# Kernel tuning notes

Hardware: AMD Instinct MI355X
Metric: run time of the kernel (lower is better)

## Reference

```python
import jax, jax.numpy as jnp
import numpy as np

# Graph geometry: L depth levels of M nodes, fan_in K scalar connections, per-node dim D
L, M, K, D, B = 8, 128, 32, 16, 2048
N = L * M  # 1024 nodes


def setup_inputs() -> dict:
    key = jax.random.key(0)
    ks = jax.random.split(key, 6)
    x = jax.random.normal(ks[0], (B, D), jnp.float32)
    trace = jax.random.normal(ks[1], (N, B, D), jnp.float32)  # previous-step recurrent state per node
    src_node = jax.random.randint(ks[2], (N, K), 0, N + 1)    # 0 = external input x, else node id (1..N)
    src_feat = jax.random.randint(ks[3], (N, K), 0, D)        # scalar index k within source output
    W = jax.random.normal(ks[4], (N, D, K), jnp.float32) / np.sqrt(K)  # per-node Linear(K -> D)
    b = jax.random.normal(ks[5], (N, D), jnp.float32) * 0.01
    return {"x": x, "trace": trace, "src_node": src_node, "src_feat": src_feat, "W": W, "b": b}


def reference(x, trace, src_node, src_feat, W, b):
    # state buffers have row 0 = external input x, rows 1..N = node states
    h_state = jnp.concatenate([jnp.zeros((1, B, D), x.dtype), jax.lax.stop_gradient(trace)], axis=0)  # prev-step snapshot (detached, like torch .detach())
    cur0 = jnp.concatenate([x[None], jax.lax.stop_gradient(trace)], axis=0)  # current-step buffer, row 0 readable as input
    sn = src_node.reshape(L, M, K)
    sf = src_feat.reshape(L, M, K)
    Wl = W.reshape(L, M, D, K)
    bl = b.reshape(L, M, D)

    def step(cur, xs):
        l, sn_l, sf_l, W_l, b_l = xs
        g_cur = cur[sn_l, :, sf_l]      # [M, K, B] gather from current-step buffer
        g_h = h_state[sn_l, :, sf_l]    # [M, K, B] gather from previous-step snapshot
        # source depth >= current depth -> recurrent edge -> read h; else feedforward -> read cur
        use_h = (sn_l > 0) & (((sn_l - 1) // M) >= l)
        g = jnp.where(use_h[:, :, None], g_h, g_cur)                     # [M, K, B]
        o = jax.nn.relu(jnp.einsum('mkb,mdk->mbd', g, W_l) + b_l[:, None, :])  # [M, B, D]
        cur = jax.lax.dynamic_update_slice(cur, o, (1 + l * M, 0, 0))    # scatter into trace buffer
        return cur, o

    _, outs = jax.lax.scan(step, cur0, (jnp.arange(L), sn, sf, Wl, bl))  # outs: [L, M, B, D]
    return outs.reshape(N, B, D)  # updated trace; last node's forward return is outs[-1]
```

## Files before the change

kernel.cpp:

```cpp
#include <hip/hip_runtime.h>
#include <hip/hip_bf16.h>

#define L_ 8
#define M_ 128
#define K_ 32
#define D_ 16
#define B_ 2048
#define N_ 1024
#define SLAB_ 32768

__global__ __launch_bounds__(256) void transpose_bd(const float* __restrict__ trace,
                                                    const float* __restrict__ x,
                                                    float* __restrict__ traceT,
                                                    float* __restrict__ xT) {
    int blk = blockIdx.x;
    const float* src;
    float* dst;
    int bt;
    if (blk < N_ * 32) {
        int n = blk >> 5;
        src = trace + (size_t)n * SLAB_;
        dst = traceT + (size_t)n * SLAB_;
        bt  = blk & 31;
    } else {
        src = x;
        dst = xT;
        bt  = blk - N_ * 32;
    }
    int b0 = bt * 64;

    __shared__ float lds[D_][65];

    int tid = threadIdx.x;

    const float4* s4 = (const float4*)src;
    int b  = tid >> 2;
    int dq = tid & 3;
    float4 v = s4[(size_t)(b0 + b) * 4 + dq];
    lds[dq * 4 + 0][b] = v.x;
    lds[dq * 4 + 1][b] = v.y;
    lds[dq * 4 + 2][b] = v.z;
    lds[dq * 4 + 3][b] = v.w;
    __syncthreads();

    int d  = tid >> 4;
    int bq = tid & 15;
    float4 w;
    w.x = lds[d][bq * 4 + 0];
    w.y = lds[d][bq * 4 + 1];
    w.z = lds[d][bq * 4 + 2];
    w.w = lds[d][bq * 4 + 3];
    ((float4*)(dst + (size_t)d * B_ + b0))[bq] = w;
}

__global__ __launch_bounds__(256) void layer_kernel(
    int l,
    const float* __restrict__ xbuf, int xfs, int xbs,
    const float* __restrict__ tbuf, int tfs, int tbs,
    const float* __restrict__ obuf, int ofs, int obs,
    const int* __restrict__ sn, const int* __restrict__ sf,
    const float* __restrict__ W, const float* __restrict__ bias,
    float* __restrict__ out, float* __restrict__ outT, int writeT)
{
    int m  = blockIdx.x >> 3;
    int bt = blockIdx.x & 7;
    int n  = l * M_ + m;
    int b  = bt * 256 + threadIdx.x;

    __shared__ float        Wsh[D_][K_];
    __shared__ float        bsh[D_];
    __shared__ const float* colp[K_];
    __shared__ int          colbs[K_];
    __shared__ float        osh[256][17];

    int tid = threadIdx.x;

    if (tid < 128) {
        ((float4*)&Wsh[0][0])[tid] = ((const float4*)(W + (size_t)n * D_ * K_))[tid];
    }
    if (tid < D_) bsh[tid] = bias[(size_t)n * D_ + tid];
    if (tid < K_) {
        int s = sn[(size_t)n * K_ + tid];
        int f = sf[(size_t)n * K_ + tid];
        const float* p;
        int bs;
        if (s == 0) {
            p  = xbuf + (size_t)f * xfs;
            bs = xbs;
        } else {
            int ls = (s - 1) >> 7;
            if (ls >= l) {
                p  = tbuf + (size_t)(s - 1) * SLAB_ + (size_t)f * tfs;
                bs = tbs;
            } else {
                p  = obuf + (size_t)(s - 1) * SLAB_ + (size_t)f * ofs;
                bs = obs;
            }
        }
        colp[tid]  = p;
        colbs[tid] = bs;
    }
    __syncthreads();

    float g[K_];
#pragma unroll
    for (int k = 0; k < K_; ++k) {
        g[k] = colp[k][(size_t)b * colbs[k]];
    }

#pragma unroll
    for (int d = 0; d < D_; ++d) {
        float acc = bsh[d];
#pragma unroll
        for (int k = 0; k < K_; ++k) acc = fmaf(g[k], Wsh[d][k], acc);
        acc = fmaxf(acc, 0.0f);
        osh[tid][d] = acc;
        if (writeT) outT[(size_t)n * SLAB_ + (size_t)d * B_ + b] = acc;
    }
    __syncthreads();

    float4* region4 = (float4*)(out + (size_t)n * SLAB_ + (size_t)(bt * 256) * D_);
#pragma unroll
    for (int j = 0; j < 4; ++j) {
        int i   = j * 256 + tid;
        int row = i >> 2;
        int c0  = (i & 3) * 4;
        float4 w;
        w.x = osh[row][c0 + 0];
        w.y = osh[row][c0 + 1];
        w.z = osh[row][c0 + 2];
        w.w = osh[row][c0 + 3];
        region4[i] = w;
    }
}

extern "C" void kernel_launch(void* const* d_in, const int* in_sizes, int n_in,
                              void* d_out, int out_size, void* d_ws, size_t ws_size,
                              hipStream_t stream) {
    const float* x     = (const float*)d_in[0];
    const float* trace = (const float*)d_in[1];
    const int*   sn    = (const int*)d_in[2];
    const int*   sf    = (const int*)d_in[3];
    const float* W     = (const float*)d_in[4];
    const float* bias  = (const float*)d_in[5];
    float*       out   = (float*)d_out;

    const size_t xT_elems  = (size_t)D_ * B_;
    const size_t big_elems = (size_t)N_ * SLAB_;
    const size_t needA = sizeof(float) * (xT_elems + 2 * big_elems);
    const size_t needB = sizeof(float) * (xT_elems + 1 * big_elems);

    float* ws = (float*)d_ws;

    if (ws_size >= needA) {
        float* xT     = ws;
        float* traceT = ws + xT_elems;
        float* outT   = traceT + big_elems;

        transpose_bd<<<N_ * 32 + 32, 256, 0, stream>>>(trace, x, traceT, xT);
        for (int l = 0; l < L_; ++l) {
            layer_kernel<<<M_ * 8, 256, 0, stream>>>(
                l,
                xT,     B_, 1,
                traceT, B_, 1,
                outT,   B_, 1,
                sn, sf, W, bias, out, outT, 1);
        }
    } else if (ws_size >= needB) {
        float* xT     = ws;
        float* traceT = ws + xT_elems;

        transpose_bd<<<N_ * 32 + 32, 256, 0, stream>>>(trace, x, traceT, xT);
        for (int l = 0; l < L_; ++l) {
            layer_kernel<<<M_ * 8, 256, 0, stream>>>(
                l,
                xT,     B_, 1,
                traceT, B_, 1,
                out,    1,  D_,
                sn, sf, W, bias, out, nullptr, 0);
        }
    } else {
        for (int l = 0; l < L_; ++l) {
            layer_kernel<<<M_ * 8, 256, 0, stream>>>(
                l,
                x,     1, D_,
                trace, 1, D_,
                out,   1, D_,
                sn, sf, W, bias, out, nullptr, 0);
        }
    }
}
```

Measured before the change: 366.7 us.

## Replace per-layer launches with one persistent kernel using per-tile dataflow flags

The eight per-layer launches are merged into a single kernel of 1024 blocks. Each block walks all layers for one node column and batch tile, and spin-waits on global per-(node, tile) ready flags only for feed-forward sources produced earlier. This removes launch gaps and whole-grid barriers between layers, letting later layers start as soon as their inputs are ready. The transpose kernel is widened to 256 batch rows per block and also clears the flags. The workspace fallback paths are removed, so the code relies on co-residency of all blocks to avoid deadlock and assumes the workspace is large enough.

New measurement: 1.263 ms. +244.3%, slower.

```diff
diff --git a/kernel.cpp b/kernel.cpp
--- a/kernel.cpp
+++ b/kernel.cpp
@@ -1,5 +1,4 @@
 #include <hip/hip_runtime.h>
-#include <hip/hip_bf16.h>
 
 #define L_ 8
 #define M_ 128
@@ -8,129 +7,158 @@
 #define B_ 2048
 #define N_ 1024
 #define SLAB_ 32768
+#define NFLAGS (N_ * 8)
 
 __global__ __launch_bounds__(256) void transpose_bd(const float* __restrict__ trace,
                                                     const float* __restrict__ x,
                                                     float* __restrict__ traceT,
-                                                    float* __restrict__ xT) {
-    int blk = blockIdx.x;
-    const float* src;
-    float* dst;
-    int bt;
-    if (blk < N_ * 32) {
-        int n = blk >> 5;
-        src = trace + (size_t)n * SLAB_;
-        dst = traceT + (size_t)n * SLAB_;
-        bt  = blk & 31;
+                                                    float* __restrict__ xT,
+                                                    int* __restrict__ flags)
+{
+    const int t   = blockIdx.x;
+    const int tid = threadIdx.x;
+    if (t < 32) flags[t * 256 + tid] = 0;
+
+    const float* src; float* dst; int bt;
+    if (t < N_ * 8) {
+        const int nn = t >> 3;
+        src = trace + (size_t)nn * SLAB_;
+        dst = traceT + (size_t)nn * SLAB_;
+        bt  = t & 7;
     } else {
-        src = x;
-        dst = xT;
-        bt  = blk - N_ * 32;
+        src = x; dst = xT; bt = t - N_ * 8;
     }
-    int b0 = bt * 64;
+    const int b0 = bt * 256;
 
-    __shared__ float lds[D_][65];
+    __shared__ float lds[16 * 257];
 
-    int tid = threadIdx.x;
-
-    const float4* s4 = (const float4*)src;
-    int b  = tid >> 2;
-    int dq = tid & 3;
-    float4 v = s4[(size_t)(b0 + b) * 4 + dq];
-    lds[dq * 4 + 0][b] = v.x;
-    lds[dq * 4 + 1][b] = v.y;
-    lds[dq * 4 + 2][b] = v.z;
-    lds[dq * 4 + 3][b] = v.w;
+    const float4* s4 = (const float4*)(src + (size_t)b0 * D_);
+    float4 v0 = s4[tid * 4 + 0];
+    float4 v1 = s4[tid * 4 + 1];
+    float4 v2 = s4[tid * 4 + 2];
+    float4 v3 = s4[tid * 4 + 3];
+    lds[ 0 * 257 + tid] = v0.x;  lds[ 1 * 257 + tid] = v0.y;
+    lds[ 2 * 257 + tid] = v0.z;  lds[ 3 * 257 + tid] = v0.w;
+    lds[ 4 * 257 + tid] = v1.x;  lds[ 5 * 257 + tid] = v1.y;
+    lds[ 6 * 257 + tid] = v1.z;  lds[ 7 * 257 + tid] = v1.w;
+    lds[ 8 * 257 + tid] = v2.x;  lds[ 9 * 257 + tid] = v2.y;
+    lds[10 * 257 + tid] = v2.z;  lds[11 * 257 + tid] = v2.w;
+    lds[12 * 257 + tid] = v3.x;  lds[13 * 257 + tid] = v3.y;
+    lds[14 * 257 + tid] = v3.z;  lds[15 * 257 + tid] = v3.w;
     __syncthreads();
 
-    int d  = tid >> 4;
-    int bq = tid & 15;
-    float4 w;
-    w.x = lds[d][bq * 4 + 0];
-    w.y = lds[d][bq * 4 + 1];
-    w.z = lds[d][bq * 4 + 2];
-    w.w = lds[d][bq * 4 + 3];
-    ((float4*)(dst + (size_t)d * B_ + b0))[bq] = w;
+    const int d  = tid >> 4;
+    const int q0 = tid & 15;
+    float* drow = dst + (size_t)d * B_ + b0;
+#pragma unroll
+    for (int j = 0; j < 4; ++j) {
+        const int bq = q0 + 16 * j;
+        float4 w;
+        w.x = lds[d * 257 + 4 * bq + 0];
+        w.y = lds[d * 257 + 4 * bq + 1];
+        w.z = lds[d * 257 + 4 * bq + 2];
+        w.w = lds[d * 257 + 4 * bq + 3];
+        ((float4*)drow)[bq] = w;
+    }
 }
 
-__global__ __launch_bounds__(256) void layer_kernel(
-    int l,
-    const float* __restrict__ xbuf, int xfs, int xbs,
-    const float* __restrict__ tbuf, int tfs, int tbs,
-    const float* __restrict__ obuf, int ofs, int obs,
+__global__ __launch_bounds__(256, 4) void layers_flag(
+    const float* __restrict__ xT, const float* __restrict__ traceT,
+    float* __restrict__ outT,
     const int* __restrict__ sn, const int* __restrict__ sf,
     const float* __restrict__ W, const float* __restrict__ bias,
-    float* __restrict__ out, float* __restrict__ outT, int writeT)
+    float* __restrict__ out, int* __restrict__ flags)
 {
-    int m  = blockIdx.x >> 3;
-    int bt = blockIdx.x & 7;
-    int n  = l * M_ + m;
-    int b  = bt * 256 + threadIdx.x;
+    const int tid = threadIdx.x;
+    const int m   = blockIdx.x >> 3;
+    const int bt  = blockIdx.x & 7;
+    const int b   = bt * 256 + tid;
 
-    __shared__ float        Wsh[D_][K_];
+    __shared__ float        Wsh[D_ * K_];
     __shared__ float        bsh[D_];
     __shared__ const float* colp[K_];
-    __shared__ int          colbs[K_];
-    __shared__ float        osh[256][17];
+    __shared__ int          waitn[K_];
+    __shared__ float        osh[256 * 17];
 
-    int tid = threadIdx.x;
+    for (int l = 0; l < L_; ++l) {
+        const int n = l * M_ + m;
 
-    if (tid < 128) {
-        ((float4*)&Wsh[0][0])[tid] = ((const float4*)(W + (size_t)n * D_ * K_))[tid];
-    }
-    if (tid < D_) bsh[tid] = bias[(size_t)n * D_ + tid];
-    if (tid < K_) {
-        int s = sn[(size_t)n * K_ + tid];
-        int f = sf[(size_t)n * K_ + tid];
-        const float* p;
-        int bs;
-        if (s == 0) {
-            p  = xbuf + (size_t)f * xfs;
-            bs = xbs;
-        } else {
-            int ls = (s - 1) >> 7;
-            if (ls >= l) {
-                p  = tbuf + (size_t)(s - 1) * SLAB_ + (size_t)f * tfs;
-                bs = tbs;
+        if (tid < 128) {
+            ((float4*)Wsh)[tid] = ((const float4*)(W + (size_t)n * D_ * K_))[tid];
+        }
+        if (tid < D_) bsh[tid] = bias[(size_t)n * D_ + tid];
+        if (tid < K_) {
+            const int s = sn[(size_t)n * K_ + tid];
+            const int f = sf[(size_t)n * K_ + tid];
+            const float* p;
+            int wn = -1;
+            if (s == 0) {
+                p = xT + (size_t)f * B_;
             } else {
-                p  = obuf + (size_t)(s - 1) * SLAB_ + (size_t)f * ofs;
-                bs = obs;
+                const int ls = (s - 1) >> 7;
+                if (ls >= l) {
+                    p = traceT + (size_t)(s - 1) * SLAB_ + (size_t)f * B_;
+                } else {
+                    p  = outT + (size_t)(s - 1) * SLAB_ + (size_t)f * B_;
+                    wn = s - 1;
+                }
+            }
+            colp[tid]  = p;
+            waitn[tid] = wn;
+        }
+        __syncthreads();
+
+        if (tid < K_) {
+            const int wn = waitn[tid];
+            if (wn >= 0) {
+                while (__hip_atomic_load(&flags[wn * 8 + bt], __ATOMIC_RELAXED,
+                                         __HIP_MEMORY_SCOPE_AGENT) == 0) {
+                    __builtin_amdgcn_s_sleep(8);
+                }
             }
         }
-        colp[tid]  = p;
-        colbs[tid] = bs;
-    }
-    __syncthreads();
+        __syncthreads();
+        __builtin_amdgcn_fence(__ATOMIC_ACQUIRE, "agent");
 
-    float g[K_];
+        float g[K_];
 #pragma unroll
-    for (int k = 0; k < K_; ++k) {
-        g[k] = colp[k][(size_t)b * colbs[k]];
-    }
+        for (int k = 0; k < K_; ++k) g[k] = colp[k][b];
 
+        const bool produce = (l < L_ - 1);
 #pragma unroll
-    for (int d = 0; d < D_; ++d) {
-        float acc = bsh[d];
+        for (int d = 0; d < D_; ++d) {
+            float acc = bsh[d];
 #pragma unroll
-        for (int k = 0; k < K_; ++k) acc = fmaf(g[k], Wsh[d][k], acc);
-        acc = fmaxf(acc, 0.0f);
-        osh[tid][d] = acc;
-        if (writeT) outT[(size_t)n * SLAB_ + (size_t)d * B_ + b] = acc;
-    }
-    __syncthreads();
+            for (int k = 0; k < K_; ++k) acc = fmaf(g[k], Wsh[d * K_ + k], acc);
+            acc = fmaxf(acc, 0.0f);
+            osh[tid * 17 + d] = acc;
+            if (produce) outT[(size_t)n * SLAB_ + (size_t)d * B_ + b] = acc;
+        }
 
-    float4* region4 = (float4*)(out + (size_t)n * SLAB_ + (size_t)(bt * 256) * D_);
+        if (produce) {
+            __builtin_amdgcn_fence(__ATOMIC_RELEASE, "agent");
+            __syncthreads();
+            if (tid == 0) {
+                __hip_atomic_store(&flags[n * 8 + bt], 1, __ATOMIC_RELAXED,
+                                   __HIP_MEMORY_SCOPE_AGENT);
+            }
+        } else {
+            __syncthreads();
+        }
+
+        float4* region4 = (float4*)(out + (size_t)n * SLAB_ + (size_t)(bt * 256) * D_);
 #pragma unroll
-    for (int j = 0; j < 4; ++j) {
-        int i   = j * 256 + tid;
-        int row = i >> 2;
-        int c0  = (i & 3) * 4;
-        float4 w;
-        w.x = osh[row][c0 + 0];
-        w.y = osh[row][c0 + 1];
-        w.z = osh[row][c0 + 2];
-        w.w = osh[row][c0 + 3];
-        region4[i] = w;
+        for (int j = 0; j < 4; ++j) {
+            const int i   = j * 256 + tid;
+            const int row = i >> 2;
+            const int c0  = (i & 3) * 4;
+            float4 w;
+            w.x = osh[row * 17 + c0 + 0];
+            w.y = osh[row * 17 + c0 + 1];
+            w.z = osh[row * 17 + c0 + 2];
+            w.w = osh[row * 17 + c0 + 3];
+            region4[i] = w;
+        }
     }
 }
 
@@ -147,46 +175,13 @@
 
     const size_t xT_elems  = (size_t)D_ * B_;
     const size_t big_elems = (size_t)N_ * SLAB_;
-    const size_t needA = sizeof(float) * (xT_elems + 2 * big_elems);
-    const size_t needB = sizeof(float) * (xT_elems + 1 * big_elems);
 
-    float* ws = (float*)d_ws;
+    float* ws     = (float*)d_ws;
+    float* xT     = ws;
+    float* traceT = ws + xT_elems;
+    float* outT   = traceT + big_elems;
+    int*   flags  = (int*)(outT + big_elems);
 
-    if (ws_size >= needA) {
-        float* xT     = ws;
-        float* traceT = ws + xT_elems;
-        float* outT   = traceT + big_elems;
-
-        transpose_bd<<<N_ * 32 + 32, 256, 0, stream>>>(trace, x, traceT, xT);
-        for (int l = 0; l < L_; ++l) {
-            layer_kernel<<<M_ * 8, 256, 0, stream>>>(
-                l,
-                xT,     B_, 1,
-                traceT, B_, 1,
-                outT,   B_, 1,
-                sn, sf, W, bias, out, outT, 1);
-        }
-    } else if (ws_size >= needB) {
-        float* xT     = ws;
-        float* traceT = ws + xT_elems;
-
-        transpose_bd<<<N_ * 32 + 32, 256, 0, stream>>>(trace, x, traceT, xT);
-        for (int l = 0; l < L_; ++l) {
-            layer_kernel<<<M_ * 8, 256, 0, stream>>>(
-                l,
-                xT,     B_, 1,
-                traceT, B_, 1,
-                out,    1,  D_,
-                sn, sf, W, bias, out, nullptr, 0);
-        }
-    } else {
-        for (int l = 0; l < L_; ++l) {
-            layer_kernel<<<M_ * 8, 256, 0, stream>>>(
-                l,
-                x,     1, D_,
-                trace, 1, D_,
-                out,   1, D_,
-                sn, sf, W, bias, out, nullptr, 0);
-        }
-    }
+    transpose_bd<<<N_ * 8 + 8, 256, 0, stream>>>(trace, x, traceT, xT, flags);
+    layers_flag<<<N_, 256, 0, stream>>>(xT, traceT, outT, sn, sf, W, bias, out, flags);
 }
```
